# Optimization experiments

Measured on AMD Instinct MI355X. Metric: run time of the kernel, lower is better.

The kernel has to match this reference:

```python
import jax, jax.numpy as jnp
import numpy as np

N_NODES = 100000
N_EDGES = 1600000
IN_F, HID, EMB = 128, 64, 32


def setup_inputs() -> dict:
    key = jax.random.key(0)
    ks = jax.random.split(key, 10)
    x = jax.random.normal(ks[0], (N_NODES, IN_F), dtype=jnp.float32)
    edge_index = jax.random.randint(ks[1], (2, N_EDGES), 0, N_NODES, dtype=jnp.int64)
    s = lambda k, sh, fan_in: jax.random.normal(k, sh, dtype=jnp.float32) / jnp.sqrt(jnp.float32(fan_in))
    return {
        "x": x,
        "edge_index": edge_index,
        # SAGEConv1: lin_l (applied to aggregated neighbors, with bias) + lin_r (root, no bias)
        "W1_l": s(ks[2], (IN_F, HID), IN_F), "b1": jnp.zeros((HID,), jnp.float32), "W1_r": s(ks[3], (IN_F, HID), IN_F),
        # SAGEConv2
        "W2_l": s(ks[4], (HID, EMB), HID), "b2": jnp.zeros((EMB,), jnp.float32), "W2_r": s(ks[5], (HID, EMB), HID),
        # risk head
        "Wh": s(ks[6], (EMB, 1), EMB), "bh": jnp.zeros((1,), jnp.float32),
    }


def _sage_conv(x, src, dst, W_l, b, W_r):
    # gather messages from source nodes, segment-mean at destination nodes
    msg_sum = jax.ops.segment_sum(x[src], dst, num_segments=N_NODES)  # [N, F]
    cnt = jax.ops.segment_sum(jnp.ones((src.shape[0],), x.dtype), dst, num_segments=N_NODES)
    mean_agg = msg_sum / jnp.maximum(cnt, 1.0)[:, None]  # isolated nodes -> 0
    return mean_agg @ W_l + b + x @ W_r


def reference(x, edge_index, W1_l, b1, W1_r, W2_l, b2, W2_r, Wh, bh):
    src, dst = edge_index[0], edge_index[1]
    h = jax.nn.relu(_sage_conv(x, src, dst, W1_l, b1, W1_r))
    # dropout is identity in eval mode
    embeddings = jax.nn.relu(_sage_conv(h, src, dst, W2_l, b2, W2_r))
    risk_scores = embeddings @ Wh + bh
    return embeddings, risk_scores
```

## Files before the change

kernel.cpp:

```cpp
#include <hip/hip_runtime.h>
#include <hip/hip_bf16.h>

#define N_NODES 100000
#define N_EDGES 1600000
#define NBUCK   196
#define BSHIFT  9
#define BCAP    12288

typedef __bf16 bf16x8 __attribute__((ext_vector_type(8)));
typedef float  f32x4  __attribute__((ext_vector_type(4)));
typedef float  f32x2  __attribute__((ext_vector_type(2)));


__device__ inline unsigned char enc_fp8(float v) {
    return (unsigned char)(__builtin_amdgcn_cvt_pk_fp8_f32(v, v, 0, 0) & 0xFF);
}

__global__ __launch_bounds__(256) void partition_k(const int* __restrict__ ei,
                                                   int* __restrict__ gcur,
                                                   unsigned* __restrict__ bbuf) {
    __shared__ int hist[NBUCK];
    __shared__ int cur[NBUCK];
    int t = threadIdx.x;
    for (int i = t; i < NBUCK; i += 256) hist[i] = 0;
    __syncthreads();
    int base = blockIdx.x * 4096;
    unsigned pk[16];
    int bk[16];
#pragma unroll
    for (int i = 0; i < 16; ++i) {
        int e = base + t + i * 256;
        if (e < N_EDGES) {
            int s = ei[e], d = ei[N_EDGES + e];
            int b = d >> BSHIFT;
            pk[i] = ((unsigned)(d & 511) << 17) | (unsigned)s;
            bk[i] = b;
            atomicAdd(&hist[b], 1);
        } else bk[i] = -1;
    }
    __syncthreads();
    for (int i = t; i < NBUCK; i += 256)
        cur[i] = atomicAdd(&gcur[i], hist[i]);
    __syncthreads();
#pragma unroll
    for (int i = 0; i < 16; ++i) {
        if (bk[i] >= 0) {
            int pos = atomicAdd(&cur[bk[i]], 1);
            bbuf[(size_t)bk[i] * BCAP + pos] = pk[i];
        }
    }
}

__global__ __launch_bounds__(256) void csr_gemm1_k(const unsigned* __restrict__ bbuf,
                                                   const int* __restrict__ gcur,
                                                   int* __restrict__ cnt,
                                                   int* __restrict__ offsets,
                                                   int* __restrict__ csr,
                                                   const float* __restrict__ x,
                                                   const float* __restrict__ W1l,
                                                   const float* __restrict__ W1r,
                                                   unsigned char* __restrict__ c1l,
                                                   __bf16* __restrict__ c1r) {
    __shared__ __align__(16) char smem[34816];
    int t = threadIdx.x;
    if (blockIdx.x < NBUCK) {
        int* lcnt = (int*)smem;
        int* loff = (int*)(smem + 2048);
        int* lcur = (int*)(smem + 4096);
        int* ssum = (int*)(smem + 6144);
        int b = blockIdx.x;
        int m = gcur[b];
        const unsigned* src = bbuf + (size_t)b * BCAP;
        for (int i = t; i < 512; i += 256) lcnt[i] = 0;
        __syncthreads();
        for (int i = t; i < m; i += 256) atomicAdd(&lcnt[src[i] >> 17], 1);
        __syncthreads();
        int a0 = lcnt[2 * t], a1 = lcnt[2 * t + 1];
        int p0 = (a0 + 3) & ~3, p1 = (a1 + 3) & ~3;
        ssum[t] = p0 + p1;
        __syncthreads();
        for (int off = 1; off < 256; off <<= 1) {
            int v = (t >= off) ? ssum[t - off] : 0;
            __syncthreads();
            ssum[t] += v;
            __syncthreads();
        }
        int ebase = (t == 0) ? 0 : ssum[t - 1];
        loff[2 * t] = ebase;
        loff[2 * t + 1] = ebase + p0;
        __syncthreads();
        for (int i = t; i < 512; i += 256) lcur[i] = loff[i];
        int nbase = b << BSHIFT;
        for (int i = t; i < 512; i += 256) {
            int n = nbase + i;
            if (n < N_NODES) {
                cnt[n] = lcnt[i];
                offsets[n] = b * BCAP + loff[i];
            }
        }
        __syncthreads();
        for (int i = t; i < m; i += 256) {
            unsigned p = src[i];
            int pos = atomicAdd(&lcur[p >> 17], 1);
            csr[(size_t)b * BCAP + pos] = (int)(p & 0x1FFFF);
        }
    } else {
        __bf16* Bt = (__bf16*)smem;
        for (int idx = t; idx < 8192; idx += 256) {
            int k = idx >> 6, n = idx & 63;
            Bt[n * 136 + k]        = (__bf16)W1l[idx];
            Bt[(n + 64) * 136 + k] = (__bf16)W1r[idx];
        }
        __syncthreads();

        int lane = t & 63, wave = t >> 6;
        int bid = blockIdx.x - NBUCK;
        int mbase = bid * 64 + wave * 16;
        int col  = lane & 15;
        int kgrp = (lane >> 4) << 3;
        int mrow = mbase + col;
        int mclamp = mrow < N_NODES ? mrow : N_NODES - 1;
        const float* arow = x + (size_t)mclamp * 128;

        f32x4 acc[8];
#pragma unroll
        for (int i = 0; i < 8; ++i) acc[i] = (f32x4){0.f, 0.f, 0.f, 0.f};

#pragma unroll
        for (int ks = 0; ks < 4; ++ks) {
            int kk = ks * 32 + kgrp;
            f32x4 a0 = *(const f32x4*)(arow + kk);
            f32x4 a1 = *(const f32x4*)(arow + kk + 4);
            bf16x8 a;
#pragma unroll
            for (int i = 0; i < 4; ++i) { a[i] = (__bf16)a0[i]; a[i + 4] = (__bf16)a1[i]; }
#pragma unroll
            for (int nt = 0; nt < 8; ++nt) {
                bf16x8 b = *(const bf16x8*)(Bt + (nt * 16 + col) * 136 + kk);
                acc[nt] = __builtin_amdgcn_mfma_f32_16x16x32_bf16(a, b, acc[nt], 0, 0, 0);
            }
        }

        int r0 = mbase + ((lane >> 4) << 2);
#pragma unroll
        for (int r = 0; r < 4; ++r) {
            int m = r0 + r;
            if (m < N_NODES) {
#pragma unroll
                for (int nt = 0; nt < 4; ++nt)
                    c1l[(size_t)m * 64 + nt * 16 + col] = enc_fp8(acc[nt][r]);
#pragma unroll
                for (int nt = 4; nt < 8; ++nt)
                    c1r[(size_t)m * 64 + (nt - 4) * 16 + col] = (__bf16)acc[nt][r];
            }
        }
    }
}

__global__ __launch_bounds__(256) void agg1_gemm2_k(const unsigned char* __restrict__ c1l,
                                                    const __bf16* __restrict__ c1r,
                                                    const int* __restrict__ offsets,
                                                    const int* __restrict__ cnt,
                                                    const int* __restrict__ csr,
                                                    const float* __restrict__ b1,
                                                    const float* __restrict__ W2l,
                                                    const float* __restrict__ W2r,
                                                    unsigned char* __restrict__ c2l,
                                                    float* __restrict__ c2r) {
    __shared__ __bf16 Bt[64 * 72];
    __shared__ __bf16 ht[64 * 72];
    int tid = threadIdx.x;
    for (int idx = tid; idx < 2048; idx += 256) {
        int k = idx >> 5, n = idx & 31;
        Bt[n * 72 + k]        = (__bf16)W2l[idx];
        Bt[(n + 32) * 72 + k] = (__bf16)W2r[idx];
    }

    int lane = tid & 63, wave = tid >> 6;
    int g = lane >> 3;
    int f8b = (lane & 7) << 3;
    f32x4 b1v0 = *(const f32x4*)(b1 + f8b);
    f32x4 b1v1 = *(const f32x4*)(b1 + f8b + 4);
    const int4* csr4 = (const int4*)csr;
#pragma unroll
    for (int p = 0; p < 2; ++p) {
        int lrow = p * 32 + wave * 8 + g;
        int n = blockIdx.x * 64 + lrow;
        bf16x8 o;
        if (n < N_NODES) {
            int beg = offsets[n], deg = cnt[n];
            int end = beg + deg;
            bf16x8 rv = *(const bf16x8*)(c1r + (size_t)n * 64 + f8b);
            float sum[8];
#pragma unroll
            for (int j = 0; j < 8; ++j) sum[j] = 0.f;
            for (int e = beg; e < end; e += 8) {
                int4 i0 = csr4[e >> 2];
                int4 i1 = csr4[(e >> 2) + 1];
                int sidx[8] = {i0.x, i0.y, i0.z, i0.w, i1.x, i1.y, i1.z, i1.w};
                uint2 w[8];
#pragma unroll
                for (int u = 0; u < 8; ++u) {
                    w[u].x = 0u; w[u].y = 0u;
                    if (e + u < end)
                        w[u] = *(const uint2*)(c1l + (size_t)sidx[u] * 64 + f8b);
                }
#pragma unroll
                for (int u = 0; u < 8; ++u) {
                    f32x2 p0 = __builtin_amdgcn_cvt_pk_f32_fp8(w[u].x, 0);
                    f32x2 p1 = __builtin_amdgcn_cvt_pk_f32_fp8(w[u].x, 1);
                    f32x2 p2 = __builtin_amdgcn_cvt_pk_f32_fp8(w[u].y, 0);
                    f32x2 p3 = __builtin_amdgcn_cvt_pk_f32_fp8(w[u].y, 1);
                    sum[0] += p0[0]; sum[1] += p0[1];
                    sum[2] += p1[0]; sum[3] += p1[1];
                    sum[4] += p2[0]; sum[5] += p2[1];
                    sum[6] += p3[0]; sum[7] += p3[1];
                }
            }
            float cf = deg > 0 ? (float)deg : 1.f;
#pragma unroll
            for (int j = 0; j < 8; ++j) {
                float v = sum[j] / cf + (float)rv[j] + ((j < 4) ? b1v0[j] : b1v1[j - 4]);
                o[j] = (__bf16)(v > 0.f ? v : 0.f);
            }
        } else {
#pragma unroll
            for (int j = 0; j < 8; ++j) o[j] = (__bf16)0.f;
        }
        *(bf16x8*)(ht + lrow * 72 + f8b) = o;
    }
    __syncthreads();

    int col  = lane & 15;
    int kgrp = (lane >> 4) << 3;
    int mbase = blockIdx.x * 64 + wave * 16;
    const __bf16* arow = ht + (wave * 16 + col) * 72;

    f32x4 acc[4];
#pragma unroll
    for (int i = 0; i < 4; ++i) acc[i] = (f32x4){0.f, 0.f, 0.f, 0.f};

#pragma unroll
    for (int ks = 0; ks < 2; ++ks) {
        int kk = ks * 32 + kgrp;
        bf16x8 a = *(const bf16x8*)(arow + kk);
#pragma unroll
        for (int nt = 0; nt < 4; ++nt) {
            bf16x8 b = *(const bf16x8*)(Bt + (nt * 16 + col) * 72 + kk);
            acc[nt] = __builtin_amdgcn_mfma_f32_16x16x32_bf16(a, b, acc[nt], 0, 0, 0);
        }
    }

    int r0 = mbase + ((lane >> 4) << 2);
#pragma unroll
    for (int r = 0; r < 4; ++r) {
        int m = r0 + r;
        if (m < N_NODES) {
#pragma unroll
            for (int nt = 0; nt < 2; ++nt)
                c2l[(size_t)m * 32 + nt * 16 + col] = enc_fp8(acc[nt][r]);
#pragma unroll
            for (int nt = 2; nt < 4; ++nt)
                c2r[(size_t)m * 32 + (nt - 2) * 16 + col] = acc[nt][r];
        }
    }
}

__global__ __launch_bounds__(256) void agg2_k(const unsigned char* __restrict__ c2l,
                                              const float* __restrict__ c2r,
                                              const int* __restrict__ offsets,
                                              const int* __restrict__ cnt,
                                              const int* __restrict__ csr,
                                              const float* __restrict__ b2,
                                              const float* __restrict__ Wh,
                                              const float* __restrict__ bh,
                                              float* __restrict__ out) {
    int wave = blockIdx.x * 4 + (threadIdx.x >> 6);
    int lane = threadIdx.x & 63;
    int g = lane >> 2;
    int n = wave * 16 + g;
    int f8b = (lane & 3) << 3;
    bool valid = n < N_NODES;
    int nc = valid ? n : N_NODES - 1;
    int beg = offsets[nc], deg = valid ? cnt[n] : 0;
    int end = beg + deg;
    f32x4 rr0 = *(const f32x4*)(c2r + (size_t)nc * 32 + f8b);
    f32x4 rr1 = *(const f32x4*)(c2r + (size_t)nc * 32 + f8b + 4);
    f32x4 wh0 = *(const f32x4*)(Wh + f8b);
    f32x4 wh1 = *(const f32x4*)(Wh + f8b + 4);
    const int4* csr4 = (const int4*)csr;
    float sum[8];
#pragma unroll
    for (int j = 0; j < 8; ++j) sum[j] = 0.f;
    for (int e = beg; e < end; e += 8) {
        int4 i0 = csr4[e >> 2];
        int4 i1 = csr4[(e >> 2) + 1];
        int sidx[8] = {i0.x, i0.y, i0.z, i0.w, i1.x, i1.y, i1.z, i1.w};
        uint2 w[8];
#pragma unroll
        for (int u = 0; u < 8; ++u) {
            w[u].x = 0u; w[u].y = 0u;
            if (e + u < end)
                w[u] = *(const uint2*)(c2l + (size_t)sidx[u] * 32 + f8b);
        }
#pragma unroll
        for (int u = 0; u < 8; ++u) {
            f32x2 p0 = __builtin_amdgcn_cvt_pk_f32_fp8(w[u].x, 0);
            f32x2 p1 = __builtin_amdgcn_cvt_pk_f32_fp8(w[u].x, 1);
            f32x2 p2 = __builtin_amdgcn_cvt_pk_f32_fp8(w[u].y, 0);
            f32x2 p3 = __builtin_amdgcn_cvt_pk_f32_fp8(w[u].y, 1);
            sum[0] += p0[0]; sum[1] += p0[1];
            sum[2] += p1[0]; sum[3] += p1[1];
            sum[4] += p2[0]; sum[5] += p2[1];
            sum[6] += p3[0]; sum[7] += p3[1];
        }
    }
    float cf = deg > 0 ? (float)deg : 1.f;
    float r = 0.f;
    f32x4 o0, o1;
#pragma unroll
    for (int j = 0; j < 8; ++j) {
        float root = (j < 4) ? rr0[j] : rr1[j - 4];
        float whj  = (j < 4) ? wh0[j] : wh1[j - 4];
        float v = sum[j] / cf + root + b2[f8b + j];
        v = v > 0.f ? v : 0.f;
        if (j < 4) o0[j] = v; else o1[j - 4] = v;
        r += v * whj;
    }
    if (valid) {
        *(f32x4*)(out + (size_t)n * 32 + f8b) = o0;
        *(f32x4*)(out + (size_t)n * 32 + f8b + 4) = o1;
    }
    r += __shfl_xor(r, 1, 64);
    r += __shfl_xor(r, 2, 64);
    if (valid && (lane & 3) == 0)
        out[(size_t)N_NODES * 32 + n] = r + bh[0];
}

extern "C" void kernel_launch(void* const* d_in, const int* in_sizes, int n_in,
                              void* d_out, int out_size, void* d_ws, size_t ws_size,
                              hipStream_t stream) {
    const float* x   = (const float*)d_in[0];
    const int*   ei  = (const int*)d_in[1];
    const float* W1l = (const float*)d_in[2];
    const float* b1  = (const float*)d_in[3];
    const float* W1r = (const float*)d_in[4];
    const float* W2l = (const float*)d_in[5];
    const float* b2  = (const float*)d_in[6];
    const float* W2r = (const float*)d_in[7];
    const float* Wh  = (const float*)d_in[8];
    const float* bh  = (const float*)d_in[9];
    float* out = (float*)d_out;

    char* ws = (char*)d_ws;
    unsigned char* c1l = (unsigned char*)(ws);
    __bf16*   c1r     = (__bf16*)(ws + 6400000);
    unsigned char* c2l = (unsigned char*)(ws + 32000000);
    float*    c2r     = (float*)(ws + 35200000);
    int*      cnt     = (int*)(ws + 48000000);
    int*      offsets = (int*)(ws + 48400000);
    int*      gcur    = (int*)(ws + 48800000);
    unsigned* bbuf    = (unsigned*)(ws + 48804096);
    int*      csr     = (int*)(ws + 58437888);

    hipMemsetAsync(gcur, 0, NBUCK * 4, stream);

    partition_k  <<<391, 256, 0, stream>>>(ei, gcur, bbuf);
    csr_gemm1_k  <<<NBUCK + 1563, 256, 0, stream>>>(bbuf, gcur, cnt, offsets, csr,
                                                    x, W1l, W1r, c1l, c1r);
    agg1_gemm2_k <<<1563, 256, 0, stream>>>(c1l, c1r, offsets, cnt, csr, b1,
                                            W2l, W2r, c2l, c2r);
    agg2_k       <<<1563, 256, 0, stream>>>(c2l, c2r, offsets, cnt, csr, b2, Wh, bh, out);
}
```

Before: 212.0 us.

## Widen per-lane gather loads, prefetch CSR indices, and halve bucket size

Both aggregation kernels now give each lane 16 features loaded as one 16-byte fp8 vector instead of 8 features at 8 bytes. This halves the number of gather instructions per edge and covers more nodes per wave, and agg2 launches half as many blocks. The CSR index loads are software-prefetched one iteration ahead. The partition now uses 391 buckets of 256 nodes, which simplifies the per-bucket scan to one node per thread. The LDS tile padding changes from 72 to 76 to reduce bank conflicts. The cost is more registers per thread and fewer lanes sharing each node's gather, which may lower occupancy; the prefetch also reads up to 8 indices past each node's segment.

Measured after the change: 212.5 us. No clear change (+0.2%).

```diff
diff --git a/kernel.cpp b/kernel.cpp
--- a/kernel.cpp
+++ b/kernel.cpp
@@ -3,9 +3,9 @@
 
 #define N_NODES 100000
 #define N_EDGES 1600000
-#define NBUCK   196
-#define BSHIFT  9
-#define BCAP    12288
+#define NBUCK   391
+#define BSHIFT  8
+#define BCAP    6144
 
 typedef __bf16 bf16x8 __attribute__((ext_vector_type(8)));
 typedef float  f32x4  __attribute__((ext_vector_type(4)));
@@ -33,7 +33,7 @@
         if (e < N_EDGES) {
             int s = ei[e], d = ei[N_EDGES + e];
             int b = d >> BSHIFT;
-            pk[i] = ((unsigned)(d & 511) << 17) | (unsigned)s;
+            pk[i] = ((unsigned)(d & 255) << 17) | (unsigned)s;
             bk[i] = b;
             atomicAdd(&hist[b], 1);
         } else bk[i] = -1;
@@ -65,19 +65,17 @@
     int t = threadIdx.x;
     if (blockIdx.x < NBUCK) {
         int* lcnt = (int*)smem;
-        int* loff = (int*)(smem + 2048);
-        int* lcur = (int*)(smem + 4096);
-        int* ssum = (int*)(smem + 6144);
+        int* lcur = (int*)(smem + 1024);
+        int* ssum = (int*)(smem + 2048);
         int b = blockIdx.x;
         int m = gcur[b];
         const unsigned* src = bbuf + (size_t)b * BCAP;
-        for (int i = t; i < 512; i += 256) lcnt[i] = 0;
+        lcnt[t] = 0;
         __syncthreads();
         for (int i = t; i < m; i += 256) atomicAdd(&lcnt[src[i] >> 17], 1);
         __syncthreads();
-        int a0 = lcnt[2 * t], a1 = lcnt[2 * t + 1];
-        int p0 = (a0 + 3) & ~3, p1 = (a1 + 3) & ~3;
-        ssum[t] = p0 + p1;
+        int a0 = lcnt[t];
+        ssum[t] = (a0 + 3) & ~3;
         __syncthreads();
         for (int off = 1; off < 256; off <<= 1) {
             int v = (t >= off) ? ssum[t - off] : 0;
@@ -86,17 +84,11 @@
             __syncthreads();
         }
         int ebase = (t == 0) ? 0 : ssum[t - 1];
-        loff[2 * t] = ebase;
-        loff[2 * t + 1] = ebase + p0;
-        __syncthreads();
-        for (int i = t; i < 512; i += 256) lcur[i] = loff[i];
-        int nbase = b << BSHIFT;
-        for (int i = t; i < 512; i += 256) {
-            int n = nbase + i;
-            if (n < N_NODES) {
-                cnt[n] = lcnt[i];
-                offsets[n] = b * BCAP + loff[i];
-            }
+        lcur[t] = ebase;
+        int n = (b << BSHIFT) + t;
+        if (n < N_NODES) {
+            cnt[n] = a0;
+            offsets[n] = b * BCAP + ebase;
         }
         __syncthreads();
         for (int i = t; i < m; i += 256) {
@@ -168,7 +160,7 @@
                                                     unsigned char* __restrict__ c2l,
                                                     float* __restrict__ c2r) {
     __shared__ __bf16 Bt[64 * 72];
-    __shared__ __bf16 ht[64 * 72];
+    __shared__ __bf16 ht[64 * 76];
     int tid = threadIdx.x;
     for (int idx = tid; idx < 2048; idx += 256) {
         int k = idx >> 5, n = idx & 31;
@@ -177,64 +169,72 @@
     }
 
     int lane = tid & 63, wave = tid >> 6;
-    int g = lane >> 3;
-    int f8b = (lane & 7) << 3;
-    f32x4 b1v0 = *(const f32x4*)(b1 + f8b);
-    f32x4 b1v1 = *(const f32x4*)(b1 + f8b + 4);
+    int g = lane >> 2;
+    int nloc = wave * 16 + g;
+    int n = blockIdx.x * 64 + nloc;
+    int f16b = (lane & 3) << 4;
+    bool valid = n < N_NODES;
+    int nc = valid ? n : N_NODES - 1;
+    int beg = offsets[nc];
+    int deg = valid ? cnt[n] : 0;
+    int end = beg + deg;
+    bf16x8 rv0 = *(const bf16x8*)(c1r + (size_t)nc * 64 + f16b);
+    bf16x8 rv1 = *(const bf16x8*)(c1r + (size_t)nc * 64 + f16b + 8);
+    f32x4 b1v[4];
+#pragma unroll
+    for (int q = 0; q < 4; ++q) b1v[q] = *(const f32x4*)(b1 + f16b + q * 4);
+
     const int4* csr4 = (const int4*)csr;
-#pragma unroll
-    for (int p = 0; p < 2; ++p) {
-        int lrow = p * 32 + wave * 8 + g;
-        int n = blockIdx.x * 64 + lrow;
-        bf16x8 o;
-        if (n < N_NODES) {
-            int beg = offsets[n], deg = cnt[n];
-            int end = beg + deg;
-            bf16x8 rv = *(const bf16x8*)(c1r + (size_t)n * 64 + f8b);
-            float sum[8];
-#pragma unroll
-            for (int j = 0; j < 8; ++j) sum[j] = 0.f;
-            for (int e = beg; e < end; e += 8) {
-                int4 i0 = csr4[e >> 2];
-                int4 i1 = csr4[(e >> 2) + 1];
-                int sidx[8] = {i0.x, i0.y, i0.z, i0.w, i1.x, i1.y, i1.z, i1.w};
-                uint2 w[8];
-#pragma unroll
-                for (int u = 0; u < 8; ++u) {
-                    w[u].x = 0u; w[u].y = 0u;
-                    if (e + u < end)
-                        w[u] = *(const uint2*)(c1l + (size_t)sidx[u] * 64 + f8b);
-                }
-#pragma unroll
-                for (int u = 0; u < 8; ++u) {
-                    f32x2 p0 = __builtin_amdgcn_cvt_pk_f32_fp8(w[u].x, 0);
-                    f32x2 p1 = __builtin_amdgcn_cvt_pk_f32_fp8(w[u].x, 1);
-                    f32x2 p2 = __builtin_amdgcn_cvt_pk_f32_fp8(w[u].y, 0);
-                    f32x2 p3 = __builtin_amdgcn_cvt_pk_f32_fp8(w[u].y, 1);
-                    sum[0] += p0[0]; sum[1] += p0[1];
-                    sum[2] += p1[0]; sum[3] += p1[1];
-                    sum[4] += p2[0]; sum[5] += p2[1];
-                    sum[6] += p3[0]; sum[7] += p3[1];
-                }
-            }
-            float cf = deg > 0 ? (float)deg : 1.f;
-#pragma unroll
-            for (int j = 0; j < 8; ++j) {
-                float v = sum[j] / cf + (float)rv[j] + ((j < 4) ? b1v0[j] : b1v1[j - 4]);
-                o[j] = (__bf16)(v > 0.f ? v : 0.f);
-            }
-        } else {
-#pragma unroll
-            for (int j = 0; j < 8; ++j) o[j] = (__bf16)0.f;
-        }
-        *(bf16x8*)(ht + lrow * 72 + f8b) = o;
-    }
+    int4 j0 = csr4[beg >> 2];
+    int4 j1 = csr4[(beg >> 2) + 1];
+    float sum[16];
+#pragma unroll
+    for (int j = 0; j < 16; ++j) sum[j] = 0.f;
+    for (int e = beg; e < end; e += 8) {
+        int4 i0 = j0, i1 = j1;
+        j0 = csr4[(e >> 2) + 2];
+        j1 = csr4[(e >> 2) + 3];
+        int sidx[8] = {i0.x, i0.y, i0.z, i0.w, i1.x, i1.y, i1.z, i1.w};
+        uint4 w[8];
+#pragma unroll
+        for (int u = 0; u < 8; ++u) {
+            w[u] = (uint4){0u, 0u, 0u, 0u};
+            if (e + u < end)
+                w[u] = *(const uint4*)(c1l + (size_t)sidx[u] * 64 + f16b);
+        }
+#pragma unroll
+        for (int u = 0; u < 8; ++u) {
+            f32x2 p0 = __builtin_amdgcn_cvt_pk_f32_fp8(w[u].x, 0);
+            f32x2 p1 = __builtin_amdgcn_cvt_pk_f32_fp8(w[u].x, 1);
+            f32x2 p2 = __builtin_amdgcn_cvt_pk_f32_fp8(w[u].y, 0);
+            f32x2 p3 = __builtin_amdgcn_cvt_pk_f32_fp8(w[u].y, 1);
+            f32x2 p4 = __builtin_amdgcn_cvt_pk_f32_fp8(w[u].z, 0);
+            f32x2 p5 = __builtin_amdgcn_cvt_pk_f32_fp8(w[u].z, 1);
+            f32x2 p6 = __builtin_amdgcn_cvt_pk_f32_fp8(w[u].w, 0);
+            f32x2 p7 = __builtin_amdgcn_cvt_pk_f32_fp8(w[u].w, 1);
+            sum[0]  += p0[0]; sum[1]  += p0[1]; sum[2]  += p1[0]; sum[3]  += p1[1];
+            sum[4]  += p2[0]; sum[5]  += p2[1]; sum[6]  += p3[0]; sum[7]  += p3[1];
+            sum[8]  += p4[0]; sum[9]  += p4[1]; sum[10] += p5[0]; sum[11] += p5[1];
+            sum[12] += p6[0]; sum[13] += p6[1]; sum[14] += p7[0]; sum[15] += p7[1];
+        }
+    }
+    float cf = deg > 0 ? (float)deg : 1.f;
+    bf16x8 o0, o1;
+#pragma unroll
+    for (int j = 0; j < 16; ++j) {
+        float rt = (j < 8) ? (float)rv0[j] : (float)rv1[j - 8];
+        float v = valid ? (sum[j] / cf + rt + b1v[j >> 2][j & 3]) : 0.f;
+        v = v > 0.f ? v : 0.f;
+        if (j < 8) o0[j] = (__bf16)v; else o1[j - 8] = (__bf16)v;
+    }
+    *(bf16x8*)(ht + nloc * 76 + f16b)     = o0;
+    *(bf16x8*)(ht + nloc * 76 + f16b + 8) = o1;
     __syncthreads();
 
     int col  = lane & 15;
     int kgrp = (lane >> 4) << 3;
     int mbase = blockIdx.x * 64 + wave * 16;
-    const __bf16* arow = ht + (wave * 16 + col) * 72;
+    const __bf16* arow = ht + (wave * 16 + col) * 76;
 
     f32x4 acc[4];
 #pragma unroll
@@ -277,31 +277,37 @@
                                               float* __restrict__ out) {
     int wave = blockIdx.x * 4 + (threadIdx.x >> 6);
     int lane = threadIdx.x & 63;
-    int g = lane >> 2;
-    int n = wave * 16 + g;
-    int f8b = (lane & 3) << 3;
+    int g = lane >> 1;
+    int n = wave * 32 + g;
+    int f16b = (lane & 1) << 4;
     bool valid = n < N_NODES;
     int nc = valid ? n : N_NODES - 1;
     int beg = offsets[nc], deg = valid ? cnt[n] : 0;
     int end = beg + deg;
-    f32x4 rr0 = *(const f32x4*)(c2r + (size_t)nc * 32 + f8b);
-    f32x4 rr1 = *(const f32x4*)(c2r + (size_t)nc * 32 + f8b + 4);
-    f32x4 wh0 = *(const f32x4*)(Wh + f8b);
-    f32x4 wh1 = *(const f32x4*)(Wh + f8b + 4);
+    f32x4 rr[4], wh[4], b2v[4];
+#pragma unroll
+    for (int q = 0; q < 4; ++q) {
+        rr[q]  = *(const f32x4*)(c2r + (size_t)nc * 32 + f16b + q * 4);
+        wh[q]  = *(const f32x4*)(Wh + f16b + q * 4);
+        b2v[q] = *(const f32x4*)(b2 + f16b + q * 4);
+    }
     const int4* csr4 = (const int4*)csr;
-    float sum[8];
-#pragma unroll
-    for (int j = 0; j < 8; ++j) sum[j] = 0.f;
+    int4 j0 = csr4[beg >> 2];
+    int4 j1 = csr4[(beg >> 2) + 1];
+    float sum[16];
+#pragma unroll
+    for (int j = 0; j < 16; ++j) sum[j] = 0.f;
     for (int e = beg; e < end; e += 8) {
-        int4 i0 = csr4[e >> 2];
-        int4 i1 = csr4[(e >> 2) + 1];
+        int4 i0 = j0, i1 = j1;
+        j0 = csr4[(e >> 2) + 2];
+        j1 = csr4[(e >> 2) + 3];
         int sidx[8] = {i0.x, i0.y, i0.z, i0.w, i1.x, i1.y, i1.z, i1.w};
-        uint2 w[8];
+        uint4 w[8];
 #pragma unroll
         for (int u = 0; u < 8; ++u) {
-            w[u].x = 0u; w[u].y = 0u;
+            w[u] = (uint4){0u, 0u, 0u, 0u};
             if (e + u < end)
-                w[u] = *(const uint2*)(c2l + (size_t)sidx[u] * 32 + f8b);
+                w[u] = *(const uint4*)(c2l + (size_t)sidx[u] * 32 + f16b);
         }
 #pragma unroll
         for (int u = 0; u < 8; ++u) {
@@ -309,31 +315,33 @@
             f32x2 p1 = __builtin_amdgcn_cvt_pk_f32_fp8(w[u].x, 1);
             f32x2 p2 = __builtin_amdgcn_cvt_pk_f32_fp8(w[u].y, 0);
             f32x2 p3 = __builtin_amdgcn_cvt_pk_f32_fp8(w[u].y, 1);
-            sum[0] += p0[0]; sum[1] += p0[1];
-            sum[2] += p1[0]; sum[3] += p1[1];
-            sum[4] += p2[0]; sum[5] += p2[1];
-            sum[6] += p3[0]; sum[7] += p3[1];
+            f32x2 p4 = __builtin_amdgcn_cvt_pk_f32_fp8(w[u].z, 0);
+            f32x2 p5 = __builtin_amdgcn_cvt_pk_f32_fp8(w[u].z, 1);
+            f32x2 p6 = __builtin_amdgcn_cvt_pk_f32_fp8(w[u].w, 0);
+            f32x2 p7 = __builtin_amdgcn_cvt_pk_f32_fp8(w[u].w, 1);
+            sum[0]  += p0[0]; sum[1]  += p0[1]; sum[2]  += p1[0]; sum[3]  += p1[1];
+            sum[4]  += p2[0]; sum[5]  += p2[1]; sum[6]  += p3[0]; sum[7]  += p3[1];
+            sum[8]  += p4[0]; sum[9]  += p4[1]; sum[10] += p5[0]; sum[11] += p5[1];
+            sum[12] += p6[0]; sum[13] += p6[1]; sum[14] += p7[0]; sum[15] += p7[1];
         }
     }
     float cf = deg > 0 ? (float)deg : 1.f;
     float r = 0.f;
-    f32x4 o0, o1;
-#pragma unroll
-    for (int j = 0; j < 8; ++j) {
-        float root = (j < 4) ? rr0[j] : rr1[j - 4];
-        float whj  = (j < 4) ? wh0[j] : wh1[j - 4];
-        float v = sum[j] / cf + root + b2[f8b + j];
+    f32x4 o[4];
+#pragma unroll
+    for (int j = 0; j < 16; ++j) {
+        float v = sum[j] / cf + rr[j >> 2][j & 3] + b2v[j >> 2][j & 3];
         v = v > 0.f ? v : 0.f;
-        if (j < 4) o0[j] = v; else o1[j - 4] = v;
-        r += v * whj;
+        o[j >> 2][j & 3] = v;
+        r += v * wh[j >> 2][j & 3];
     }
     if (valid) {
-        *(f32x4*)(out + (size_t)n * 32 + f8b) = o0;
-        *(f32x4*)(out + (size_t)n * 32 + f8b + 4) = o1;
+#pragma unroll
+        for (int q = 0; q < 4; ++q)
+            *(f32x4*)(out + (size_t)n * 32 + f16b + q * 4) = o[q];
     }
     r += __shfl_xor(r, 1, 64);
-    r += __shfl_xor(r, 2, 64);
-    if (valid && (lane & 3) == 0)
+    if (valid && (lane & 1) == 0)
         out[(size_t)N_NODES * 32 + n] = r + bh[0];
 }
 
@@ -370,5 +378,5 @@
                                                     x, W1l, W1r, c1l, c1r);
     agg1_gemm2_k <<<1563, 256, 0, stream>>>(c1l, c1r, offsets, cnt, csr, b1,
                                             W2l, W2r, c2l, c2r);
-    agg2_k       <<<1563, 256, 0, stream>>>(c2l, c2r, offsets, cnt, csr, b2, Wh, bh, out);
-}
+    agg2_k       <<<782, 256, 0, stream>>>(c2l, c2r, offsets, cnt, csr, b2, Wh, bh, out);
+}
```
